# Kernel tuning notes

Measured on AMD Instinct MI355X. Metric: run time of the kernel, lower is better.

Reference implementation:

```python
import jax, jax.numpy as jnp
import numpy as np
from jax import lax

BITWIDTH = 7
EPS = 1e-5


def ti_quant(x):
    """TiFloatToInt8: per-tensor int8 quantization with power-of-2 scale."""
    rng = jnp.max(jnp.abs(x))
    bw = jnp.ceil(jnp.log2(rng))
    exp = bw - BITWIDTH
    q = jnp.clip(jnp.round(x * 2.0 ** (BITWIDTH - bw)), -128.0, 127.0)
    return q, exp


def ti_conv(xv, xe, wv, we, pad):
    """TiConv2d: integer conv (simulated in f32, all values int-valued),
    int32 accumulate, then shift back to 8 bits; exponents add."""
    acc = lax.conv_general_dilated(
        xv, wv, window_strides=(1, 1), padding=[(pad, pad), (pad, pad)],
        dimension_numbers=("NCHW", "OIHW", "NCHW"))
    rng = jnp.max(jnp.abs(acc))
    bw = jnp.ceil(jnp.log2(rng))
    shift = jnp.maximum(bw - BITWIDTH, 0.0)
    q = jnp.clip(jnp.round(acc * 2.0 ** (-shift)), -128.0, 127.0)
    return q, xe + we + shift


def batchnorm(x, gamma, beta):
    # training-mode BN: batch statistics over (N, H, W)
    mean = jnp.mean(x, axis=(0, 2, 3), keepdims=True)
    var = jnp.var(x, axis=(0, 2, 3), keepdims=True)
    g = gamma[None, :, None, None]
    b = beta[None, :, None, None]
    return g * (x - mean) * lax.rsqrt(var + EPS) + b


def setup_inputs() -> dict:
    key = jax.random.key(0)
    k0, k1, k2, k3, k4 = jax.random.split(key, 5)
    B, Cin, Cout, H, W = 32, 128, 256, 56, 56
    x_val = jax.random.randint(k0, (B, Cin, H, W), -128, 128, dtype=jnp.int32)
    x_exp = jnp.zeros((), jnp.float32) - 7.0
    wDW = jnp.round(jnp.clip(jax.random.normal(k1, (Cin, Cin, 3, 3), jnp.float32) * 32.0, -128.0, 127.0))
    wDW_exp = jnp.zeros((), jnp.float32) - 9.0
    wPW = jnp.round(jnp.clip(jax.random.normal(k2, (Cout, Cin, 1, 1), jnp.float32) * 32.0, -128.0, 127.0))
    wPW_exp = jnp.zeros((), jnp.float32) - 9.0
    gamma1 = jnp.ones((Cin,), jnp.float32) + 0.1 * jax.random.normal(k3, (Cin,), jnp.float32)
    beta1 = jnp.zeros((Cin,), jnp.float32)
    gamma2 = jnp.ones((Cout,), jnp.float32) + 0.1 * jax.random.normal(k4, (Cout,), jnp.float32)
    beta2 = jnp.zeros((Cout,), jnp.float32)
    return {"x_val": x_val, "x_exp": x_exp, "wDW": wDW, "wDW_exp": wDW_exp,
            "wPW": wPW, "wPW_exp": wPW_exp, "gamma1": gamma1, "beta1": beta1,
            "gamma2": gamma2, "beta2": beta2}


def reference(x_val, x_exp, wDW, wDW_exp, wPW, wPW_exp, gamma1, beta1, gamma2, beta2):
    xv = x_val.astype(jnp.float32)
    # convDW (3x3, in->in, pad=1)
    q, e = ti_conv(xv, x_exp, wDW, wDW_exp, 1)
    # dequant -> bn1 -> quant
    f = batchnorm(q * 2.0 ** e, gamma1, beta1)
    q, e = ti_quant(f)
    # TiReLU on int values
    q = jnp.maximum(q, 0.0)
    # convPW (1x1, in->out)
    q, e = ti_conv(q, e, wPW, wPW_exp, 0)
    # dequant -> bn2 -> quant -> relu
    f = batchnorm(q * 2.0 ** e, gamma2, beta2)
    q, e = ti_quant(f)
    q = jnp.maximum(q, 0.0)
    return q.astype(jnp.int8), e
```

## Files before the change

### kernel.cpp

```cpp
#include <hip/hip_runtime.h>
#include <cstdint>
#include <cstddef>

#define C1 128
#define C2 256
#define Hh 56
#define Wd 56
#define HW 3136
#define NHW 100352
#define N1 ((size_t)12845056)
#define N2 ((size_t)25690112)
#define XPSZ ((size_t)13778944)

typedef int v4i __attribute__((ext_vector_type(4)));
typedef int v16i __attribute__((ext_vector_type(16)));

static constexpr size_t OFF_XP = 0;
static constexpr size_t OFF_Q1 = XPSZ;
static constexpr size_t OFF_Q3 = OFF_Q1 + N1;
static constexpr size_t OFF_WQ1 = OFF_Q3 + N2;
static constexpr size_t OFF_WQ2 = OFF_WQ1 + 147456;
static constexpr size_t OFF_STATS = OFF_WQ2 + 32768;

struct Stats {
  int absmax1, absmax2, pad0, pad1;
  float scale1, e1, s2, e2;
  float scaleq2, e3, sf, ef;
  long long sum1[C1];
  unsigned long long sumsq1[C1];
  int min1[C1], max1[C1];
  float A1[C1], B1c[C1];
  long long sum2[C2];
  unsigned long long sumsq2[C2];
  int min2[C2], max2[C2];
  float A2[C2], B2c[C2];
};

__global__ void k_init(Stats* st) {
  int t = threadIdx.x;
  if (t == 0) { st->absmax1 = 0; st->absmax2 = 0; }
  for (int c = t; c < C1; c += 256) {
    st->sum1[c] = 0; st->sumsq1[c] = 0; st->min1[c] = 127; st->max1[c] = -128;
  }
  for (int c = t; c < C2; c += 256) {
    st->sum2[c] = 0; st->sumsq2[c] = 0; st->min2[c] = 127; st->max2[c] = -128;
  }
}

__global__ __launch_bounds__(256) void k_prep_x2(
    const int* __restrict__ x, signed char* __restrict__ xp) {
  __shared__ signed char lds[56 * 132];
  int t = threadIdx.x;
  int hh = blockIdx.x;
  int n = blockIdx.y;
  int* xpw = (int*)(xp + ((size_t)n * 58 + hh) * 7424);
  if (hh == 0 || hh == 57) {
    for (int o = t; o < 1856; o += 256) xpw[o] = 0;
    return;
  }
  int h = hh - 1;
  const int* xb = x + (size_t)n * C1 * HW + h * 56;
  for (int idx = t; idx < 7168; idx += 256) {
    int c = idx / 56, w = idx - c * 56;
    lds[w * 132 + c] = (signed char)xb[(size_t)c * HW + w];
  }
  __syncthreads();
  for (int o = t; o < 1856; o += 256) {
    int kb = o / 232, r = o - kb * 232, ww = r >> 2, cw = r & 3;
    int val = (ww == 0 || ww == 57) ? 0
              : *(const int*)&lds[(ww - 1) * 132 + kb * 16 + cw * 4];
    xpw[o] = val;
  }
}

__global__ void k_prep_w1(const float* __restrict__ wDW, signed char* __restrict__ wq1t) {
  int idx = blockIdx.x * 256 + threadIdx.x;
  if (idx >= 128 * 1152) return;
  int co = idx / 1152, r = idx - co * 1152;
  int ci = r / 9, pos = r - ci * 9;
  int k = pos * 128 + ci;
  wq1t[(size_t)(k >> 4) * 2048 + co * 16 + (k & 15)] = (signed char)(int)wDW[idx];
}

__global__ void k_prep_w2(const float* __restrict__ wPW, signed char* __restrict__ wq2t) {
  int i = blockIdx.x * 256 + threadIdx.x;
  int co = i >> 7, ci = i & 127;
  wq2t[(size_t)(ci >> 4) * 4096 + co * 16 + (ci & 15)] = (signed char)(int)wPW[i];
}

__global__ void k_scale(const int* __restrict__ absmax_p,
                        const float* __restrict__ ea, const float* __restrict__ eb,
                        float* scale_out, float* e_out) {
  int v = *absmax_p;
  int p = 31 - __clz(v | 1);
  int bw = ((v & (v - 1)) == 0) ? p : p + 1;
  int shift = bw - 7; if (shift < 0) shift = 0;
  *scale_out = exp2f((float)(-shift));
  *e_out = *ea + *eb + (float)shift;
}

__device__ inline v4i ld16_lds(const signed char* p) {
  const int2* q = (const int2*)p;
  int2 lo = q[0], hi = q[1];
  v4i r; r[0] = lo.x; r[1] = lo.y; r[2] = hi.x; r[3] = hi.y;
  return r;
}

template <int STORE>
__global__ __launch_bounds__(256, 2) void k_conv1t(
    const signed char* __restrict__ xp, const signed char* __restrict__ wq1t,
    signed char* __restrict__ q1, Stats* st) {
  __shared__ int qti[256 * 34];
  __shared__ int psum[C1], psq[C1], pmn[C1], pmx[C1];
  __shared__ int reda[4];
  signed char* qt = (signed char*)qti;

  int t = threadIdx.x, lane = t & 63, wave = t >> 6;
  int half = lane >> 5, l31 = lane & 31;
  size_t g0 = (size_t)blockIdx.x * 256;

  const signed char* ab[2];
#pragma unroll
  for (int i = 0; i < 2; ++i) {
    size_t gm = g0 + wave * 64 + i * 32 + l31;
    int n = (int)(gm / HW);
    int p = (int)(gm - (size_t)n * HW);
    int h = p / 56, w = p - h * 56;
    ab[i] = xp + ((size_t)n * 58 + h) * 7424 + w * 16 + half * 928;
  }
  const signed char* bb[4];
#pragma unroll
  for (int j = 0; j < 4; ++j)
    bb[j] = wq1t + (size_t)(j * 32 + l31) * 16 + half * 2048;

  v16i a1[2][4];
#pragma unroll
  for (int i = 0; i < 2; ++i)
#pragma unroll
    for (int j = 0; j < 4; ++j)
#pragma unroll
      for (int r = 0; r < 16; ++r) a1[i][j][r] = 0;

#pragma unroll
  for (int pos = 0; pos < 9; ++pos) {
    int kh = pos / 3, kw = pos - kh * 3;
    const signed char* a0p = ab[0] + kh * 7424 + kw * 16;
    const signed char* a1p = ab[1] + kh * 7424 + kw * 16;
#pragma unroll
    for (int kb = 0; kb < 8; kb += 2) {
      v4i af0 = *(const v4i*)(a0p + kb * 928);
      v4i af1 = *(const v4i*)(a1p + kb * 928);
      v4i bf[4];
#pragma unroll
      for (int j = 0; j < 4; ++j)
        bf[j] = *(const v4i*)(bb[j] + pos * 16384 + kb * 2048);
#pragma unroll
      for (int j = 0; j < 4; ++j) {
        a1[0][j] = __builtin_amdgcn_mfma_i32_32x32x32_i8(af0, bf[j], a1[0][j], 0, 0, 0);
        a1[1][j] = __builtin_amdgcn_mfma_i32_32x32x32_i8(af1, bf[j], a1[1][j], 0, 0, 0);
      }
    }
  }

  if (STORE == 0) {
    int am = 0;
#pragma unroll
    for (int i = 0; i < 2; ++i)
#pragma unroll
      for (int j = 0; j < 4; ++j)
#pragma unroll
        for (int r = 0; r < 16; ++r) am = max(am, abs(a1[i][j][r]));
    for (int off = 32; off; off >>= 1) am = max(am, __shfl_down(am, off, 64));
    if (lane == 0) reda[wave] = am;
    __syncthreads();
    if (t == 0)
      atomicMax(&st->absmax1, max(max(reda[0], reda[1]), max(reda[2], reda[3])));
  } else {
    if (t < C1) { psum[t] = 0; psq[t] = 0; pmn[t] = 127; pmx[t] = -128; }
    __syncthreads();
    float scale1 = st->scale1;
#pragma unroll
    for (int j = 0; j < 4; ++j) {
      int sj = 0, sqj = 0, mnj = 127, mxj = -128;
      int c = j * 32 + l31;
#pragma unroll
      for (int i = 0; i < 2; ++i)
#pragma unroll
        for (int reg = 0; reg < 16; ++reg) {
          int row = (reg & 3) + 8 * (reg >> 2) + 4 * half;
          int pix = wave * 64 + i * 32 + row;
          float r = rintf((float)a1[i][j][reg] * scale1);
          r = fminf(fmaxf(r, -128.f), 127.f);
          int qi = (int)r;
          qt[pix * 136 + c] = (signed char)qi;
          sj += qi; sqj += qi * qi; mnj = min(mnj, qi); mxj = max(mxj, qi);
        }
      sj += __shfl_down(sj, 32, 64);
      sqj += __shfl_down(sqj, 32, 64);
      mnj = min(mnj, __shfl_down(mnj, 32, 64));
      mxj = max(mxj, __shfl_down(mxj, 32, 64));
      if (half == 0) {
        atomicAdd(&psum[c], sj); atomicAdd(&psq[c], sqj);
        atomicMin(&pmn[c], mnj); atomicMax(&pmx[c], mxj);
      }
    }
    __syncthreads();
    if (t < C1) {
      atomicAdd((unsigned long long*)&st->sum1[t],
                (unsigned long long)(long long)psum[t]);
      atomicAdd(&st->sumsq1[t], (unsigned long long)(unsigned)psq[t]);
      atomicMin(&st->min1[t], pmn[t]);
      atomicMax(&st->max1[t], pmx[t]);
    }
    int* q1w = (int*)(q1 + g0 * 128);
    for (int idx = t; idx < 8192; idx += 256) {
      int pix = idx >> 5, c4 = idx & 31;
      q1w[idx] = qti[pix * 34 + c4];
    }
  }
}

template <int STORE>
__global__ __launch_bounds__(256, 2) void k_conv2t(
    const signed char* __restrict__ q1, const signed char* __restrict__ wq2t,
    signed char* __restrict__ q3, Stats* st) {
  __shared__ int qti[256 * 34];
  __shared__ int psum[C2], psq[C2], pmn[C2], pmx[C2];
  __shared__ int reda[4];
  signed char* qt = (signed char*)qti;

  int t = threadIdx.x, lane = t & 63, wave = t >> 6;
  int half = lane >> 5, l31 = lane & 31;
  size_t g0 = (size_t)blockIdx.x * 256;

  if (STORE) {
    psum[t] = 0; psq[t] = 0; pmn[t] = 127; pmx[t] = -128;
  }
  int c4 = t & 31;
  float Av[4], Bv[4];
#pragma unroll
  for (int jj = 0; jj < 4; ++jj) {
    Av[jj] = st->A1[c4 * 4 + jj];
    Bv[jj] = st->B1c[c4 * 4 + jj];
  }
  float s2 = st->s2;
  const int* q1w = (const int*)(q1 + g0 * 128);
#pragma unroll
  for (int k = 0; k < 32; ++k) {
    int idx = k * 256 + t;
    int v = q1w[idx];
    int pix = idx >> 5;
    int outv = 0;
#pragma unroll
    for (int jj = 0; jj < 4; ++jj) {
      int b = (signed char)(v >> (8 * jj));
      float y = Av[jj] * (float)b + Bv[jj];
      float r = rintf(y * s2);
      r = fminf(fmaxf(r, -128.f), 127.f);
      r = fmaxf(r, 0.f);
      outv |= ((int)r & 0xff) << (8 * jj);
    }
    qti[pix * 34 + c4] = outv;
  }
  __syncthreads();

  float scale2 = STORE ? st->scaleq2 : 0.f;
  int am2 = 0;
#pragma unroll
  for (int ch = 0; ch < 2; ++ch) {
    v16i a2[2][4];
#pragma unroll
    for (int i = 0; i < 2; ++i)
#pragma unroll
      for (int j = 0; j < 4; ++j)
#pragma unroll
        for (int r = 0; r < 16; ++r) a2[i][j][r] = 0;
#pragma unroll
    for (int ks = 0; ks < 4; ++ks) {
      v4i af[2];
#pragma unroll
      for (int i = 0; i < 2; ++i)
        af[i] = ld16_lds(&qt[(wave * 64 + i * 32 + l31) * 136 + half * 16 + ks * 32]);
      v4i bf[4];
#pragma unroll
      for (int j = 0; j < 4; ++j)
        bf[j] = *(const v4i*)(wq2t + (size_t)(ks * 2 + half) * 4096 +
                              (ch * 128 + j * 32 + l31) * 16);
#pragma unroll
      for (int j = 0; j < 4; ++j) {
        a2[0][j] = __builtin_amdgcn_mfma_i32_32x32x32_i8(af[0], bf[j], a2[0][j], 0, 0, 0);
        a2[1][j] = __builtin_amdgcn_mfma_i32_32x32x32_i8(af[1], bf[j], a2[1][j], 0, 0, 0);
      }
    }
    if (STORE == 0) {
#pragma unroll
      for (int i = 0; i < 2; ++i)
#pragma unroll
        for (int j = 0; j < 4; ++j)
#pragma unroll
          for (int r = 0; r < 16; ++r) am2 = max(am2, abs(a2[i][j][r]));
    } else {
#pragma unroll
      for (int j = 0; j < 4; ++j) {
        int sj = 0, sqj = 0, mnj = 127, mxj = -128;
        int c = ch * 128 + j * 32 + l31;
#pragma unroll
        for (int i = 0; i < 2; ++i)
#pragma unroll
          for (int reg = 0; reg < 16; ++reg) {
            int row = (reg & 3) + 8 * (reg >> 2) + 4 * half;
            size_t g = g0 + wave * 64 + i * 32 + row;
            float r = rintf((float)a2[i][j][reg] * scale2);
            r = fminf(fmaxf(r, -128.f), 127.f);
            int qi = (int)r;
            q3[g * 256 + c] = (signed char)qi;
            sj += qi; sqj += qi * qi; mnj = min(mnj, qi); mxj = max(mxj, qi);
          }
        sj += __shfl_down(sj, 32, 64);
        sqj += __shfl_down(sqj, 32, 64);
        mnj = min(mnj, __shfl_down(mnj, 32, 64));
        mxj = max(mxj, __shfl_down(mxj, 32, 64));
        if (half == 0) {
          atomicAdd(&psum[c], sj); atomicAdd(&psq[c], sqj);
          atomicMin(&pmn[c], mnj); atomicMax(&pmx[c], mxj);
        }
      }
    }
  }
  if (STORE == 0) {
    for (int off = 32; off; off >>= 1) am2 = max(am2, __shfl_down(am2, off, 64));
    if (lane == 0) reda[wave] = am2;
    __syncthreads();
    if (t == 0)
      atomicMax(&st->absmax2, max(max(reda[0], reda[1]), max(reda[2], reda[3])));
  } else {
    __syncthreads();
    atomicAdd((unsigned long long*)&st->sum2[t],
              (unsigned long long)(long long)psum[t]);
    atomicAdd(&st->sumsq2[t], (unsigned long long)(unsigned)psq[t]);
    atomicMin(&st->min2[t], pmn[t]);
    atomicMax(&st->max2[t], pmx[t]);
  }
}

__global__ void k_bn(const long long* __restrict__ sums,
                     const unsigned long long* __restrict__ sumsqs,
                     const int* __restrict__ mins, const int* __restrict__ maxs,
                     const float* __restrict__ gamma, const float* __restrict__ beta,
                     const float* __restrict__ e_in,
                     float* A, float* Bc, float* s_out, float* e_out,
                     float* e_extra, int C) {
  __shared__ float red[4];
  int t = threadIdx.x;
  float e1 = *e_in;
  double meanq = (double)sums[t] / (double)NHW;
  double varq = (double)sumsqs[t] / (double)NHW - meanq * meanq;
  float se = exp2f(e1);
  float mean = (float)meanq * se;
  float var = (float)varq * se * se;
  float rsq = 1.0f / sqrtf(var + 1e-5f);
  float g = gamma[t], b = beta[t];
  float Avv = g * se * rsq;
  float Bvv = b - g * mean * rsq;
  A[t] = Avv; Bc[t] = Bvv;
  float cand = fmaxf(fabsf(Avv * (float)mins[t] + Bvv), fabsf(Avv * (float)maxs[t] + Bvv));
  for (int off = 32; off; off >>= 1) cand = fmaxf(cand, __shfl_down(cand, off, 64));
  int wave = t >> 6, lane = t & 63;
  if (lane == 0) red[wave] = cand;
  __syncthreads();
  if (t == 0) {
    float rng = red[0];
    for (int i = 1; i < C / 64; i++) rng = fmaxf(rng, red[i]);
    float bwv = ceilf(log2f(rng));
    *s_out = exp2f(7.0f - bwv);
    *e_out = bwv - 7.0f;
    if (e_extra) *e_extra = bwv - 7.0f;
  }
}

__global__ __launch_bounds__(256) void k_out(
    const signed char* __restrict__ q3, const Stats* __restrict__ st,
    float* __restrict__ out) {
  int t = threadIdx.x, lane = t & 63, wave = t >> 6;
  int nb = blockIdx.x;
  int n = nb / 49, p0 = (nb - n * 49) * 64;
  const int* q3w = (const int*)(q3 + ((size_t)n * HW + p0) * 256);
  float sf = st->sf;
  float* ob = out + (size_t)n * C2 * HW + p0 + lane;
#pragma unroll
  for (int i = 0; i < 16; ++i) {
    int cg2 = wave * 16 + i;
    int v = q3w[(size_t)lane * 64 + cg2];
#pragma unroll
    for (int j = 0; j < 4; ++j) {
      int c = cg2 * 4 + j;
      float y = st->A2[c] * (float)((signed char)(v >> (8 * j))) + st->B2c[c];
      float r = rintf(y * sf);
      r = fminf(fmaxf(r, -128.f), 127.f);
      ob[(size_t)c * HW] = fmaxf(r, 0.f);
    }
  }
}

extern "C" void kernel_launch(void* const* d_in, const int* in_sizes, int n_in,
                              void* d_out, int out_size, void* d_ws, size_t ws_size,
                              hipStream_t stream) {
  const int* x = (const int*)d_in[0];
  const float* x_exp = (const float*)d_in[1];
  const float* wDW = (const float*)d_in[2];
  const float* wDW_exp = (const float*)d_in[3];
  const float* wPW = (const float*)d_in[4];
  const float* wPW_exp = (const float*)d_in[5];
  const float* gamma1 = (const float*)d_in[6];
  const float* beta1 = (const float*)d_in[7];
  const float* gamma2 = (const float*)d_in[8];
  const float* beta2 = (const float*)d_in[9];
  float* out = (float*)d_out;

  char* ws = (char*)d_ws;
  signed char* xp2 = (signed char*)(ws + OFF_XP);
  signed char* q1 = (signed char*)(ws + OFF_Q1);
  signed char* q3 = (signed char*)(ws + OFF_Q3);
  signed char* wq1t = (signed char*)(ws + OFF_WQ1);
  signed char* wq2t = (signed char*)(ws + OFF_WQ2);
  Stats* st = (Stats*)(ws + OFF_STATS);

  hipLaunchKernelGGL(k_init, dim3(1), dim3(256), 0, stream, st);
  hipLaunchKernelGGL(k_prep_x2, dim3(58, 32), dim3(256), 0, stream, x, xp2);
  hipLaunchKernelGGL(k_prep_w1, dim3(576), dim3(256), 0, stream, wDW, wq1t);
  hipLaunchKernelGGL(k_prep_w2, dim3(128), dim3(256), 0, stream, wPW, wq2t);

  hipLaunchKernelGGL(k_conv1t<0>, dim3(392), dim3(256), 0, stream,
                     xp2, wq1t, q1, st);
  hipLaunchKernelGGL(k_scale, dim3(1), dim3(1), 0, stream,
                     &st->absmax1, x_exp, wDW_exp, &st->scale1, &st->e1);
  hipLaunchKernelGGL(k_conv1t<1>, dim3(392), dim3(256), 0, stream,
                     xp2, wq1t, q1, st);
  hipLaunchKernelGGL(k_bn, dim3(1), dim3(C1), 0, stream,
                     st->sum1, st->sumsq1, st->min1, st->max1, gamma1, beta1,
                     &st->e1, st->A1, st->B1c, &st->s2, &st->e2, (float*)nullptr, C1);

  hipLaunchKernelGGL(k_conv2t<0>, dim3(392), dim3(256), 0, stream,
                     q1, wq2t, q3, st);
  hipLaunchKernelGGL(k_scale, dim3(1), dim3(1), 0, stream,
                     &st->absmax2, &st->e2, wPW_exp, &st->scaleq2, &st->e3);
  hipLaunchKernelGGL(k_conv2t<1>, dim3(392), dim3(256), 0, stream,
                     q1, wq2t, q3, st);
  hipLaunchKernelGGL(k_bn, dim3(1), dim3(C2), 0, stream,
                     st->sum2, st->sumsq2, st->min2, st->max2, gamma2, beta2,
                     &st->e3, st->A2, st->B2c, &st->sf, &st->ef, out + N2, C2);
  hipLaunchKernelGGL(k_out, dim3(1568), dim3(256), 0, stream, q3, st, out);
}
```

Before: 312.9 us.

## Stage conv2 outputs in LDS for coalesced stores and retile to 128 pixels

The pointwise conv kernel now processes 128 pixels per block with all 256 output channels per wave. Quantized outputs are written to an LDS staging buffer and then stored to global memory as coalesced 32-bit words, replacing scattered byte stores. BN statistic accumulators shrink from 64-bit to 32-bit atomics. The trade-offs are more LDS per block, which may limit occupancy, and reliance on the sums fitting in 32 bits.

```diff
diff --git a/kernel.cpp b/kernel.cpp
--- a/kernel.cpp
+++ b/kernel.cpp
@@ -26,12 +26,10 @@
   int absmax1, absmax2, pad0, pad1;
   float scale1, e1, s2, e2;
   float scaleq2, e3, sf, ef;
-  long long sum1[C1];
-  unsigned long long sumsq1[C1];
+  int sum1[C1]; unsigned sumsq1[C1];
   int min1[C1], max1[C1];
   float A1[C1], B1c[C1];
-  long long sum2[C2];
-  unsigned long long sumsq2[C2];
+  int sum2[C2]; unsigned sumsq2[C2];
   int min2[C2], max2[C2];
   float A2[C2], B2c[C2];
 };
@@ -206,9 +204,8 @@
     }
     __syncthreads();
     if (t < C1) {
-      atomicAdd((unsigned long long*)&st->sum1[t],
-                (unsigned long long)(long long)psum[t]);
-      atomicAdd(&st->sumsq1[t], (unsigned long long)(unsigned)psq[t]);
+      atomicAdd(&st->sum1[t], psum[t]);
+      atomicAdd(&st->sumsq1[t], (unsigned)psq[t]);
       atomicMin(&st->min1[t], pmn[t]);
       atomicMax(&st->max1[t], pmx[t]);
     }
@@ -224,18 +221,18 @@
 __global__ __launch_bounds__(256, 2) void k_conv2t(
     const signed char* __restrict__ q1, const signed char* __restrict__ wq2t,
     signed char* __restrict__ q3, Stats* st) {
-  __shared__ int qti[256 * 34];
+  __shared__ int qti[128 * 34];
+  __shared__ signed char stg[128 * 264];
   __shared__ int psum[C2], psq[C2], pmn[C2], pmx[C2];
   __shared__ int reda[4];
   signed char* qt = (signed char*)qti;
 
   int t = threadIdx.x, lane = t & 63, wave = t >> 6;
   int half = lane >> 5, l31 = lane & 31;
-  size_t g0 = (size_t)blockIdx.x * 256;
-
-  if (STORE) {
-    psum[t] = 0; psq[t] = 0; pmn[t] = 127; pmx[t] = -128;
-  }
+  size_t g0 = (size_t)blockIdx.x * 128;
+
+  if (STORE) { psum[t] = 0; psq[t] = 0; pmn[t] = 127; pmx[t] = -128; }
+
   int c4 = t & 31;
   float Av[4], Bv[4];
 #pragma unroll
@@ -246,7 +243,7 @@
   float s2 = st->s2;
   const int* q1w = (const int*)(q1 + g0 * 128);
 #pragma unroll
-  for (int k = 0; k < 32; ++k) {
+  for (int k = 0; k < 16; ++k) {
     int idx = k * 256 + t;
     int v = q1w[idx];
     int pix = idx >> 5;
@@ -264,87 +261,74 @@
   }
   __syncthreads();
 
-  float scale2 = STORE ? st->scaleq2 : 0.f;
-  int am2 = 0;
-#pragma unroll
-  for (int ch = 0; ch < 2; ++ch) {
-    v16i a2[2][4];
-#pragma unroll
-    for (int i = 0; i < 2; ++i)
-#pragma unroll
-      for (int j = 0; j < 4; ++j)
-#pragma unroll
-        for (int r = 0; r < 16; ++r) a2[i][j][r] = 0;
-#pragma unroll
-    for (int ks = 0; ks < 4; ++ks) {
-      v4i af[2];
-#pragma unroll
-      for (int i = 0; i < 2; ++i)
-        af[i] = ld16_lds(&qt[(wave * 64 + i * 32 + l31) * 136 + half * 16 + ks * 32]);
-      v4i bf[4];
-#pragma unroll
-      for (int j = 0; j < 4; ++j)
-        bf[j] = *(const v4i*)(wq2t + (size_t)(ks * 2 + half) * 4096 +
-                              (ch * 128 + j * 32 + l31) * 16);
-#pragma unroll
-      for (int j = 0; j < 4; ++j) {
-        a2[0][j] = __builtin_amdgcn_mfma_i32_32x32x32_i8(af[0], bf[j], a2[0][j], 0, 0, 0);
-        a2[1][j] = __builtin_amdgcn_mfma_i32_32x32x32_i8(af[1], bf[j], a2[1][j], 0, 0, 0);
-      }
-    }
-    if (STORE == 0) {
-#pragma unroll
-      for (int i = 0; i < 2; ++i)
-#pragma unroll
-        for (int j = 0; j < 4; ++j)
-#pragma unroll
-          for (int r = 0; r < 16; ++r) am2 = max(am2, abs(a2[i][j][r]));
-    } else {
-#pragma unroll
-      for (int j = 0; j < 4; ++j) {
-        int sj = 0, sqj = 0, mnj = 127, mxj = -128;
-        int c = ch * 128 + j * 32 + l31;
-#pragma unroll
-        for (int i = 0; i < 2; ++i)
-#pragma unroll
-          for (int reg = 0; reg < 16; ++reg) {
-            int row = (reg & 3) + 8 * (reg >> 2) + 4 * half;
-            size_t g = g0 + wave * 64 + i * 32 + row;
-            float r = rintf((float)a2[i][j][reg] * scale2);
-            r = fminf(fmaxf(r, -128.f), 127.f);
-            int qi = (int)r;
-            q3[g * 256 + c] = (signed char)qi;
-            sj += qi; sqj += qi * qi; mnj = min(mnj, qi); mxj = max(mxj, qi);
-          }
-        sj += __shfl_down(sj, 32, 64);
-        sqj += __shfl_down(sqj, 32, 64);
-        mnj = min(mnj, __shfl_down(mnj, 32, 64));
-        mxj = max(mxj, __shfl_down(mxj, 32, 64));
-        if (half == 0) {
-          atomicAdd(&psum[c], sj); atomicAdd(&psq[c], sqj);
-          atomicMin(&pmn[c], mnj); atomicMax(&pmx[c], mxj);
-        }
-      }
-    }
-  }
+  v16i acc[8];
+#pragma unroll
+  for (int j = 0; j < 8; ++j)
+#pragma unroll
+    for (int r = 0; r < 16; ++r) acc[j][r] = 0;
+
+#pragma unroll
+  for (int ks = 0; ks < 4; ++ks) {
+    v4i af = ld16_lds(&qt[(wave * 32 + l31) * 136 + half * 16 + ks * 32]);
+#pragma unroll
+    for (int j = 0; j < 8; ++j) {
+      v4i bf = *(const v4i*)(wq2t + (size_t)(ks * 2 + half) * 4096 + (j * 32 + l31) * 16);
+      acc[j] = __builtin_amdgcn_mfma_i32_32x32x32_i8(af, bf, acc[j], 0, 0, 0);
+    }
+  }
+
   if (STORE == 0) {
+    int am2 = 0;
+#pragma unroll
+    for (int j = 0; j < 8; ++j)
+#pragma unroll
+      for (int r = 0; r < 16; ++r) am2 = max(am2, abs(acc[j][r]));
     for (int off = 32; off; off >>= 1) am2 = max(am2, __shfl_down(am2, off, 64));
     if (lane == 0) reda[wave] = am2;
     __syncthreads();
     if (t == 0)
       atomicMax(&st->absmax2, max(max(reda[0], reda[1]), max(reda[2], reda[3])));
   } else {
+    float scale2 = st->scaleq2;
+#pragma unroll
+    for (int j = 0; j < 8; ++j) {
+      int c = j * 32 + l31;
+      int sj = 0, sqj = 0, mnj = 127, mxj = -128;
+#pragma unroll
+      for (int reg = 0; reg < 16; ++reg) {
+        int row = (reg & 3) + 8 * (reg >> 2) + 4 * half;
+        float r = rintf((float)acc[j][reg] * scale2);
+        r = fminf(fmaxf(r, -128.f), 127.f);
+        int qi = (int)r;
+        stg[(wave * 32 + row) * 264 + c] = (signed char)qi;
+        sj += qi; sqj += qi * qi; mnj = min(mnj, qi); mxj = max(mxj, qi);
+      }
+      sj += __shfl_down(sj, 32, 64);
+      sqj += __shfl_down(sqj, 32, 64);
+      mnj = min(mnj, __shfl_down(mnj, 32, 64));
+      mxj = max(mxj, __shfl_down(mxj, 32, 64));
+      if (half == 0) {
+        atomicAdd(&psum[c], sj); atomicAdd(&psq[c], sqj);
+        atomicMin(&pmn[c], mnj); atomicMax(&pmx[c], mxj);
+      }
+    }
     __syncthreads();
-    atomicAdd((unsigned long long*)&st->sum2[t],
-              (unsigned long long)(long long)psum[t]);
-    atomicAdd(&st->sumsq2[t], (unsigned long long)(unsigned)psq[t]);
+    atomicAdd(&st->sum2[t], psum[t]);
+    atomicAdd(&st->sumsq2[t], (unsigned)psq[t]);
     atomicMin(&st->min2[t], pmn[t]);
     atomicMax(&st->max2[t], pmx[t]);
-  }
-}
-
-__global__ void k_bn(const long long* __restrict__ sums,
-                     const unsigned long long* __restrict__ sumsqs,
+    int* q3w = (int*)(q3 + g0 * 256);
+#pragma unroll
+    for (int k = 0; k < 32; ++k) {
+      int idx = k * 256 + t;
+      int pix = idx >> 6, cw = idx & 63;
+      q3w[idx] = *(const int*)&stg[pix * 264 + cw * 4];
+    }
+  }
+}
+
+__global__ void k_bn(const int* __restrict__ sums,
+                     const unsigned* __restrict__ sumsqs,
                      const int* __restrict__ mins, const int* __restrict__ maxs,
                      const float* __restrict__ gamma, const float* __restrict__ beta,
                      const float* __restrict__ e_in,
@@ -440,11 +424,11 @@
                      st->sum1, st->sumsq1, st->min1, st->max1, gamma1, beta1,
                      &st->e1, st->A1, st->B1c, &st->s2, &st->e2, (float*)nullptr, C1);
 
-  hipLaunchKernelGGL(k_conv2t<0>, dim3(392), dim3(256), 0, stream,
+  hipLaunchKernelGGL(k_conv2t<0>, dim3(784), dim3(256), 0, stream,
                      q1, wq2t, q3, st);
   hipLaunchKernelGGL(k_scale, dim3(1), dim3(1), 0, stream,
                      &st->absmax2, &st->e2, wPW_exp, &st->scaleq2, &st->e3);
-  hipLaunchKernelGGL(k_conv2t<1>, dim3(392), dim3(256), 0, stream,
+  hipLaunchKernelGGL(k_conv2t<1>, dim3(784), dim3(256), 0, stream,
                      q1, wq2t, q3, st);
   hipLaunchKernelGGL(k_bn, dim3(1), dim3(C2), 0, stream,
                      st->sum2, st->sumsq2, st->min2, st->max2, gamma2, beta2,
```

Result: no change. 315.7 us (+0.9%).
